# Optimization experiments

Hardware: AMD Instinct MI355X
Metric: run time of the kernel (lower is better)

## Reference

```python
import jax, jax.numpy as jnp
import numpy as np

EPSILON = 1e-15
LOG2 = 0.6931471805599453
N_VARS = 4096
BATCH = 512
OUT_SIZES = [16384, 8192, 4096, 2048]
FANINS = [4, 2, 4, 2]


def log1mexp(x):
    # accurate log(1 - exp(x)) for x < 0
    return jnp.where(x > -LOG2,
                     jnp.log(-jnp.expm1(x)),
                     jnp.log1p(-jnp.exp(x)))


def encode_input(pos):
    # rows: [-inf, 0, pos0, neg0, pos1, neg1, ...]
    neg = log1mexp(pos)
    inter = jnp.stack([pos, neg], axis=1).reshape(2 * pos.shape[0], pos.shape[1])
    head = jnp.stack([jnp.full(pos.shape[1:], -jnp.inf, pos.dtype),
                      jnp.zeros(pos.shape[1:], pos.dtype)])
    return jnp.concatenate([head, inter], axis=0)


def product_layer(x, ptrs, seg, n_out):
    return jax.ops.segment_sum(x[ptrs], seg, num_segments=n_out)


def sum_layer(x, ptrs, seg, n_out):
    g = x[ptrs]
    a = jax.lax.stop_gradient(jax.ops.segment_max(g, seg, num_segments=n_out))
    s = jax.ops.segment_sum(jnp.exp(g - a[seg]), seg, num_segments=n_out)
    return jnp.log(s + EPSILON) + a


def setup_inputs() -> dict:
    rng = np.random.default_rng(0)
    # log-probabilities in (-inf, 0): pos = log(u), u in (0,1)
    u = rng.uniform(1e-4, 1.0 - 1e-4, size=(N_VARS, BATCH)).astype(np.float32)
    x = jnp.asarray(np.log(u))

    inputs = {"x": x}
    prev_size = 2 * N_VARS + 2
    for i, (n_out, fanin) in enumerate(zip(OUT_SIZES, FANINS)):
        n_edges = n_out * fanin
        lo = 1 if i == 0 else 0  # avoid the -inf constant row at layer 0
        ptrs = rng.integers(lo, prev_size, size=n_edges).astype(np.int64)
        seg = np.repeat(np.arange(n_out, dtype=np.int64), fanin)
        inputs[f"ptrs{i}"] = jnp.asarray(ptrs)
        inputs[f"seg{i}"] = jnp.asarray(seg)
        prev_size = n_out
    return inputs


def reference(x, ptrs0, seg0, ptrs1, seg1, ptrs2, seg2, ptrs3, seg3):
    h = encode_input(x)
    ptrs = [ptrs0, ptrs1, ptrs2, ptrs3]
    segs = [seg0, seg1, seg2, seg3]
    for i, n_out in enumerate(OUT_SIZES):
        if i % 2 == 0:
            h = product_layer(h, ptrs[i], segs[i], n_out)
        else:
            h = sum_layer(h, ptrs[i], segs[i], n_out)
    return h
```

## Files before the change

### kernel.cpp

```cpp
#include <hip/hip_runtime.h>
#include <math.h>

#define BATCH    512
#define N_VARS   4096
#define H_ROWS   (2 * N_VARS + 2)
#define N_OUT1   8192
#define N_OUT3   2048
#define TPB      1024

__device__ __forceinline__ float log1mexp_fast(float x) {
    return __logf(1.0f - __expf(x));
}

__device__ __forceinline__ float lse2_fast(float a, float b) {
    float m = fmaxf(a, b);
    float d = fabsf(a - b);
    return m + __logf(1.0f + __expf(-d));
}

__global__ void build_tab_kernel(const int* __restrict__ p_prod,
                                 const int* __restrict__ p_sum,
                                 int4* __restrict__ tab, int n_out) {
    int o = blockIdx.x * blockDim.x + threadIdx.x;
    if (o >= n_out) return;
    int2 pp = ((const int2*)p_sum)[o];
    tab[2 * o]     = ((const int4*)p_prod)[pp.x];
    tab[2 * o + 1] = ((const int4*)p_prod)[pp.y];
}

#define TDIM 32
__global__ void transpose_kernel(const float* __restrict__ in,
                                 float* __restrict__ out, int R, int C) {
    __shared__ float tile[TDIM][TDIM + 1];
    int cb = blockIdx.x * TDIM;
    int rb = blockIdx.y * TDIM;
    int tx = threadIdx.x, ty = threadIdx.y;
#pragma unroll
    for (int j = 0; j < TDIM; j += 8)
        tile[ty + j][tx] = in[(size_t)(rb + ty + j) * C + cb + tx];
    __syncthreads();
#pragma unroll
    for (int j = 0; j < TDIM; j += 8)
        out[(size_t)(cb + ty + j) * R + rb + tx] = tile[tx][ty + j];
}

__global__ void __launch_bounds__(TPB, 8)
fused_spn_kernel(const float* __restrict__ xT,
                 const int4* __restrict__ tabB,
                 const int4* __restrict__ tabC,
                 float* __restrict__ outT) {
    __shared__ float buf[H_ROWS];
    const int b = blockIdx.x;
    const int t = threadIdx.x;

    if (t == 0) { buf[0] = -INFINITY; buf[1] = 0.f; }
    {
        float4 p = ((const float4*)(xT + (size_t)b * N_VARS))[t];
        int base = 8 * t + 2;
        buf[base + 0] = p.x;  buf[base + 1] = log1mexp_fast(p.x);
        buf[base + 2] = p.y;  buf[base + 3] = log1mexp_fast(p.y);
        buf[base + 4] = p.z;  buf[base + 5] = log1mexp_fast(p.z);
        buf[base + 6] = p.w;  buf[base + 7] = log1mexp_fast(p.w);
    }
    __syncthreads();

    float r1[N_OUT1 / TPB];
#pragma unroll
    for (int c = 0; c < N_OUT1 / TPB; c += 4) {
        int4 qa[4], qb[4];
#pragma unroll
        for (int k = 0; k < 4; ++k) {
            int o = t + (c + k) * TPB;
            qa[k] = tabB[2 * o];
            qb[k] = tabB[2 * o + 1];
        }
#pragma unroll
        for (int k = 0; k < 4; ++k) {
            float ga = buf[qa[k].x] + buf[qa[k].y] + buf[qa[k].z] + buf[qa[k].w];
            float gb = buf[qb[k].x] + buf[qb[k].y] + buf[qb[k].z] + buf[qb[k].w];
            r1[c + k] = lse2_fast(ga, gb);
        }
    }
    __syncthreads();
#pragma unroll
    for (int k = 0; k < N_OUT1 / TPB; ++k)
        buf[t + k * TPB] = r1[k];
    __syncthreads();

    {
        int4 qa[2], qb[2];
#pragma unroll
        for (int k = 0; k < 2; ++k) {
            int o = t + k * TPB;
            qa[k] = tabC[2 * o];
            qb[k] = tabC[2 * o + 1];
        }
#pragma unroll
        for (int k = 0; k < 2; ++k) {
            int o = t + k * TPB;
            float ga = buf[qa[k].x] + buf[qa[k].y] + buf[qa[k].z] + buf[qa[k].w];
            float gb = buf[qb[k].x] + buf[qb[k].y] + buf[qb[k].z] + buf[qb[k].w];
            outT[(size_t)b * N_OUT3 + o] = lse2_fast(ga, gb);
        }
    }
}

extern "C" void kernel_launch(void* const* d_in, const int* in_sizes, int n_in,
                              void* d_out, int out_size, void* d_ws, size_t ws_size,
                              hipStream_t stream) {
    const float* x     = (const float*)d_in[0];
    const int*   ptrs0 = (const int*)d_in[1];
    const int*   ptrs1 = (const int*)d_in[3];
    const int*   ptrs2 = (const int*)d_in[5];
    const int*   ptrs3 = (const int*)d_in[7];
    float* out = (float*)d_out;

    float* xT   = (float*)d_ws;
    float* outT = xT + (size_t)N_VARS * BATCH;
    int4*  tabB = (int4*)(outT + (size_t)N_OUT3 * BATCH);
    int4*  tabC = tabB + 2 * N_OUT1;

    build_tab_kernel<<<N_OUT1 / 256, 256, 0, stream>>>(ptrs0, ptrs1, tabB, N_OUT1);
    build_tab_kernel<<<N_OUT3 / 256, 256, 0, stream>>>(ptrs2, ptrs3, tabC, N_OUT3);

    transpose_kernel<<<dim3(BATCH / TDIM, N_VARS / TDIM), dim3(32, 8), 0, stream>>>(
        x, xT, N_VARS, BATCH);

    fused_spn_kernel<<<BATCH, TPB, 0, stream>>>(xT, tabB, tabC, outT);

    transpose_kernel<<<dim3(N_OUT3 / TDIM, BATCH / TDIM), dim3(32, 8), 0, stream>>>(
        outT, out, BATCH, N_OUT3);
}
```

Measured before the change: 95.86 us.

## Process two batch columns per block with float2 shared buffer and merge table kernels

Result: faster. 91.74 us (-4.3%).

```diff
diff --git a/kernel.cpp b/kernel.cpp
--- a/kernel.cpp
+++ b/kernel.cpp
@@ -7,25 +7,37 @@
 #define N_OUT1   8192
 #define N_OUT3   2048
 #define TPB      1024
+#define SMEM_BYTES (H_ROWS * sizeof(float2))
 
 __device__ __forceinline__ float log1mexp_fast(float x) {
     return __logf(1.0f - __expf(x));
 }
 
-__device__ __forceinline__ float lse2_fast(float a, float b) {
-    float m = fmaxf(a, b);
-    float d = fabsf(a - b);
-    return m + __logf(1.0f + __expf(-d));
+__device__ __forceinline__ float2 lse2_fast2(float2 a, float2 b) {
+    float2 r;
+    float mx = fmaxf(a.x, b.x), my = fmaxf(a.y, b.y);
+    r.x = mx + __logf(1.0f + __expf(-fabsf(a.x - b.x)));
+    r.y = my + __logf(1.0f + __expf(-fabsf(a.y - b.y)));
+    return r;
 }
 
-__global__ void build_tab_kernel(const int* __restrict__ p_prod,
-                                 const int* __restrict__ p_sum,
-                                 int4* __restrict__ tab, int n_out) {
+__global__ void build_tabs_kernel(const int* __restrict__ p0,
+                                  const int* __restrict__ p1,
+                                  const int* __restrict__ p2,
+                                  const int* __restrict__ p3,
+                                  int4* __restrict__ tabB,
+                                  int4* __restrict__ tabC) {
     int o = blockIdx.x * blockDim.x + threadIdx.x;
-    if (o >= n_out) return;
-    int2 pp = ((const int2*)p_sum)[o];
-    tab[2 * o]     = ((const int4*)p_prod)[pp.x];
-    tab[2 * o + 1] = ((const int4*)p_prod)[pp.y];
+    if (o < N_OUT1) {
+        int2 pp = ((const int2*)p1)[o];
+        tabB[2 * o]     = ((const int4*)p0)[pp.x];
+        tabB[2 * o + 1] = ((const int4*)p0)[pp.y];
+    } else {
+        int oc = o - N_OUT1;
+        int2 pp = ((const int2*)p3)[oc];
+        tabC[2 * oc]     = ((const int4*)p2)[pp.x];
+        tabC[2 * oc + 1] = ((const int4*)p2)[pp.y];
+    }
 }
 
 #define TDIM 32
@@ -44,27 +56,36 @@
         out[(size_t)(cb + ty + j) * R + rb + tx] = tile[tx][ty + j];
 }
 
-__global__ void __launch_bounds__(TPB, 8)
+__global__ void __launch_bounds__(TPB, 4)
 fused_spn_kernel(const float* __restrict__ xT,
                  const int4* __restrict__ tabB,
                  const int4* __restrict__ tabC,
                  float* __restrict__ outT) {
-    __shared__ float buf[H_ROWS];
-    const int b = blockIdx.x;
+    extern __shared__ float2 buf[];
+    const int b0 = 2 * blockIdx.x;
+    const int b1 = b0 + 1;
     const int t = threadIdx.x;
 
-    if (t == 0) { buf[0] = -INFINITY; buf[1] = 0.f; }
+    if (t == 0) {
+        buf[0] = make_float2(-INFINITY, -INFINITY);
+        buf[1] = make_float2(0.f, 0.f);
+    }
     {
-        float4 p = ((const float4*)(xT + (size_t)b * N_VARS))[t];
+        float4 pa = ((const float4*)(xT + (size_t)b0 * N_VARS))[t];
+        float4 pb = ((const float4*)(xT + (size_t)b1 * N_VARS))[t];
         int base = 8 * t + 2;
-        buf[base + 0] = p.x;  buf[base + 1] = log1mexp_fast(p.x);
-        buf[base + 2] = p.y;  buf[base + 3] = log1mexp_fast(p.y);
-        buf[base + 4] = p.z;  buf[base + 5] = log1mexp_fast(p.z);
-        buf[base + 6] = p.w;  buf[base + 7] = log1mexp_fast(p.w);
+        buf[base + 0] = make_float2(pa.x, pb.x);
+        buf[base + 1] = make_float2(log1mexp_fast(pa.x), log1mexp_fast(pb.x));
+        buf[base + 2] = make_float2(pa.y, pb.y);
+        buf[base + 3] = make_float2(log1mexp_fast(pa.y), log1mexp_fast(pb.y));
+        buf[base + 4] = make_float2(pa.z, pb.z);
+        buf[base + 5] = make_float2(log1mexp_fast(pa.z), log1mexp_fast(pb.z));
+        buf[base + 6] = make_float2(pa.w, pb.w);
+        buf[base + 7] = make_float2(log1mexp_fast(pa.w), log1mexp_fast(pb.w));
     }
     __syncthreads();
 
-    float r1[N_OUT1 / TPB];
+    float2 r1[N_OUT1 / TPB];
 #pragma unroll
     for (int c = 0; c < N_OUT1 / TPB; c += 4) {
         int4 qa[4], qb[4];
@@ -76,9 +97,15 @@
         }
 #pragma unroll
         for (int k = 0; k < 4; ++k) {
-            float ga = buf[qa[k].x] + buf[qa[k].y] + buf[qa[k].z] + buf[qa[k].w];
-            float gb = buf[qb[k].x] + buf[qb[k].y] + buf[qb[k].z] + buf[qb[k].w];
-            r1[c + k] = lse2_fast(ga, gb);
+            float2 va0 = buf[qa[k].x], va1 = buf[qa[k].y];
+            float2 va2 = buf[qa[k].z], va3 = buf[qa[k].w];
+            float2 vb0 = buf[qb[k].x], vb1 = buf[qb[k].y];
+            float2 vb2 = buf[qb[k].z], vb3 = buf[qb[k].w];
+            float2 ga = make_float2(va0.x + va1.x + va2.x + va3.x,
+                                    va0.y + va1.y + va2.y + va3.y);
+            float2 gb = make_float2(vb0.x + vb1.x + vb2.x + vb3.x,
+                                    vb0.y + vb1.y + vb2.y + vb3.y);
+            r1[c + k] = lse2_fast2(ga, gb);
         }
     }
     __syncthreads();
@@ -98,9 +125,17 @@
 #pragma unroll
         for (int k = 0; k < 2; ++k) {
             int o = t + k * TPB;
-            float ga = buf[qa[k].x] + buf[qa[k].y] + buf[qa[k].z] + buf[qa[k].w];
-            float gb = buf[qb[k].x] + buf[qb[k].y] + buf[qb[k].z] + buf[qb[k].w];
-            outT[(size_t)b * N_OUT3 + o] = lse2_fast(ga, gb);
+            float2 va0 = buf[qa[k].x], va1 = buf[qa[k].y];
+            float2 va2 = buf[qa[k].z], va3 = buf[qa[k].w];
+            float2 vb0 = buf[qb[k].x], vb1 = buf[qb[k].y];
+            float2 vb2 = buf[qb[k].z], vb3 = buf[qb[k].w];
+            float2 ga = make_float2(va0.x + va1.x + va2.x + va3.x,
+                                    va0.y + va1.y + va2.y + va3.y);
+            float2 gb = make_float2(vb0.x + vb1.x + vb2.x + vb3.x,
+                                    vb0.y + vb1.y + vb2.y + vb3.y);
+            float2 r = lse2_fast2(ga, gb);
+            outT[(size_t)b0 * N_OUT3 + o] = r.x;
+            outT[(size_t)b1 * N_OUT3 + o] = r.y;
         }
     }
 }
@@ -120,13 +155,20 @@
     int4*  tabB = (int4*)(outT + (size_t)N_OUT3 * BATCH);
     int4*  tabC = tabB + 2 * N_OUT1;
 
-    build_tab_kernel<<<N_OUT1 / 256, 256, 0, stream>>>(ptrs0, ptrs1, tabB, N_OUT1);
-    build_tab_kernel<<<N_OUT3 / 256, 256, 0, stream>>>(ptrs2, ptrs3, tabC, N_OUT3);
+    static bool attr_set = false;
+    if (!attr_set) {
+        hipFuncSetAttribute((const void*)fused_spn_kernel,
+                            hipFuncAttributeMaxDynamicSharedMemorySize, SMEM_BYTES);
+        attr_set = true;
+    }
+
+    build_tabs_kernel<<<(N_OUT1 + N_OUT3) / 256, 256, 0, stream>>>(
+        ptrs0, ptrs1, ptrs2, ptrs3, tabB, tabC);
 
     transpose_kernel<<<dim3(BATCH / TDIM, N_VARS / TDIM), dim3(32, 8), 0, stream>>>(
         x, xT, N_VARS, BATCH);
 
-    fused_spn_kernel<<<BATCH, TPB, 0, stream>>>(xT, tabB, tabC, outT);
+    fused_spn_kernel<<<BATCH / 2, TPB, SMEM_BYTES, stream>>>(xT, tabB, tabC, outT);
 
     transpose_kernel<<<dim3(N_OUT3 / TDIM, BATCH / TDIM), dim3(32, 8), 0, stream>>>(
         outT, out, BATCH, N_OUT3);
```
